# Performance work log

Measured on AMD Instinct MI355X. Metric: run time of the kernel, lower is better.

## Reference

```python
import jax, jax.numpy as jnp
import numpy as np

# ---- static config (mirrors init_kwargs + fixed setup box dims) ----
PC_MIN = jnp.array([0.0, -40.0, -3.0])
VOXEL_SIZE = jnp.array([0.05, 0.05, 0.1])
STRIDE = 4                     # pool_cfg.STRIDE and multi_scale_3d_strides['x_conv4']
EXTEND = 2.0                   # model_cfg.ROI_EXTEND_FACTOR
GRID_ZYX = (10, 400, 352)      # sparse spatial shape after stride-4 downsample [z,y,x]
# grid_size = round(extended_dims / voxel_size / STRIDE) for fixed dims [6.4,3.2,1.6]
GX, GY, GZ = 64, 32, 4
G = GX * GY * GZ
N_VOX, C = 200_000, 128
M = 64
KX, KY, KZ = 7, 7, 3


def setup_inputs() -> dict:
    key = jax.random.key(0)
    k1, k2, k3, k4, k5, k6, k7, k8, k9 = jax.random.split(key, 9)
    ctr = jnp.stack([
        jax.random.uniform(k1, (M,), minval=10.0, maxval=60.0),
        jax.random.uniform(k2, (M,), minval=-25.0, maxval=25.0),
        jax.random.uniform(k3, (M,), minval=-1.5, maxval=0.5)], axis=-1)
    dims = jnp.tile(jnp.array([[6.4, 3.2, 1.6]], jnp.float32), (M, 1))  # fixed -> static grid
    yaw = jax.random.uniform(k4, (M, 1), minval=-np.pi, maxval=np.pi)
    rois = jnp.concatenate([ctr, dims, yaw], axis=-1).astype(jnp.float32)
    proto_box = jnp.array([0.0, 0.0, 0.0, 6.4, 3.2, 1.6, 0.3], jnp.float32)
    voxel_feats = jax.random.normal(k5, (N_VOX, C), jnp.float32)
    feat_proto = jax.random.normal(k6, (1, KX, KY, KZ, C), jnp.float32) * 0.1
    zc = jax.random.randint(k7, (N_VOX,), 0, GRID_ZYX[0])
    yc = jax.random.randint(k8, (N_VOX,), 0, GRID_ZYX[1])
    xc = jax.random.randint(k9, (N_VOX,), 0, GRID_ZYX[2])
    voxel_coords = jnp.stack([jnp.zeros_like(zc), zc, yc, xc], -1).astype(jnp.int32)
    return dict(rois=rois, proto_box=proto_box, voxel_feats=voxel_feats,
                feat_proto=feat_proto, voxel_coords=voxel_coords)


def _dense_grid_points(box):
    # get_dense_grid_points: row-major (x,y,z) index order, matches torch nonzero()
    idx = jnp.stack(jnp.meshgrid(jnp.arange(GX), jnp.arange(GY), jnp.arange(GZ),
                                 indexing='ij'), -1).reshape(-1, 3).astype(jnp.float32)
    gs = jnp.array([GX, GY, GZ], jnp.float32)
    return (idx + 0.5) / gs * box[3:6] - box[3:6] / 2.0  # (G,3)


def _rotate_z(pts, ang):
    # common_utils.rotate_points_along_z: pts @ [[c,s,0],[-s,c,0],[0,0,1]]
    c, s = jnp.cos(ang), jnp.sin(ang)
    R = jnp.stack([jnp.stack([c, s, 0.0 * c]),
                   jnp.stack([-s, c, 0.0 * c]),
                   jnp.stack([0.0 * c, 0.0 * c, 1.0 + 0.0 * c])])
    return pts @ R


def reference(rois, proto_box, voxel_feats, feat_proto, voxel_coords):
    # generate_voxel2pinds: dense [Z,Y,X] grid of voxel row indices, -1 = empty
    v2p = -jnp.ones(GRID_ZYX, jnp.int32)
    v2p = v2p.at[voxel_coords[:, 1], voxel_coords[:, 2], voxel_coords[:, 3]].set(
        jnp.arange(N_VOX, dtype=jnp.int32))

    def per_roi(box):
        box = box.at[3:5].multiply(EXTEND)                 # xy_dim_extend
        local = _dense_grid_points(box)                    # (G,3)
        xyz = _rotate_z(local, box[6]) + box[:3]           # global roi grid points
        coords = jnp.floor((xyz - PC_MIN) / VOXEL_SIZE)    # '//' floor-div semantics
        coords = jnp.floor(coords / STRIDE).astype(jnp.int32)
        xc, yc, zc = coords[:, 0], coords[:, 1], coords[:, 2]
        inb = ((zc >= 0) & (zc < GRID_ZYX[0]) & (yc >= 0) & (yc < GRID_ZYX[1]) &
               (xc >= 0) & (xc < GRID_ZYX[2]))
        pidx = v2p[jnp.clip(zc, 0, GRID_ZYX[0] - 1),
                   jnp.clip(yc, 0, GRID_ZYX[1] - 1),
                   jnp.clip(xc, 0, GRID_ZYX[2] - 1)]
        valid = inb & (pidx >= 0)
        feat = jnp.where(valid[:, None], voxel_feats[jnp.clip(pidx, 0)], 0.0)  # (G,C)
        return feat, xyz

    feats, grid_xyz = jax.vmap(per_roi)(rois)              # (M,G,C), (M,G,3)
    vol = feats.reshape(M, GX, GY, GZ, C).transpose(0, 4, 1, 2, 3)   # NCDHW
    kern = feat_proto.transpose(0, 4, 1, 2, 3)                        # (1,C,KX,KY,KZ)
    pads = [(KX // 2,) * 2, (KY // 2,) * 2, (KZ // 2,) * 2]           # ceil((k-1)/2)
    mm = jax.lax.conv_general_dilated(vol, kern, (1, 1, 1), pads,
                                      dimension_numbers=('NCDHW', 'OIDHW', 'NCDHW'))
    # fresh BatchNorm3d(1) applied per-ROI (batch 1 each call): per-sample norm
    mu = jnp.mean(mm, axis=(1, 2, 3, 4), keepdims=True)
    var = jnp.var(mm, axis=(1, 2, 3, 4), keepdims=True)
    mm = (mm - mu) / jnp.sqrt(var + 1e-5)
    idx = jnp.minimum(jnp.argmax(mm.reshape(M, -1), axis=1), G - 1)
    sel = jnp.take_along_axis(grid_xyz, idx[:, None, None], axis=1)[:, 0, :]  # (M,3)
    rois_new = jnp.tile(proto_box[None], (M, 1))
    rois_new = rois_new.at[:, :3].set(sel)
    return rois_new
```

## Files before the change

### kernel.cpp

```cpp
#include <hip/hip_runtime.h>
#include <stdint.h>

#define GRID_Z 10
#define GRID_Y 400
#define GRID_X 352
#define NGRID (GRID_Z * GRID_Y * GRID_X)
#define NVOX 200000
#define CCH 128
#define MROI 64
#define GXD 64
#define GYD 32
#define GZD 4
#define GCELLS 8192
#define NTAPS 147
#define TROWS 32
#define NSLC 12
#define PITCH 136
#define NTT 10
#define BFRAGN (NTT * 4 * 64)
#define VCLR ((NGRID / 4 + 255) / 256)
#define ABLK 16

typedef short bf16x8 __attribute__((ext_vector_type(8)));
typedef float f32x4 __attribute__((ext_vector_type(4)));

__device__ __forceinline__ unsigned f2bf(float x) {
    unsigned u = __float_as_uint(x);
    return (u + 0x7FFFu + ((u >> 16) & 1u)) >> 16;
}
__device__ __forceinline__ float bf2f(unsigned h) {
    return __uint_as_float(h << 16);
}

__device__ __forceinline__ void cell_xyz(const float* __restrict__ roi, int g,
                                         float& X, float& Y, float& Z) {
#pragma clang fp contract(off)
    int iz = g & 3;
    int iy = (g >> 2) & 31;
    int ix = g >> 7;
    float bx = roi[3] * 2.0f;
    float by = roi[4] * 2.0f;
    float bz = roi[5];
    float lx = (ix + 0.5f) / 64.0f * bx - bx / 2.0f;
    float ly = (iy + 0.5f) / 32.0f * by - by / 2.0f;
    float lz = (iz + 0.5f) / 4.0f  * bz - bz / 2.0f;
    float c = cosf(roi[6]);
    float s = sinf(roi[6]);
    X = lx * c + ly * (-s) + roi[0];
    Y = lx * s + ly * c    + roi[1];
    Z = lz + roi[2];
}

__global__ void k_prep(const float* __restrict__ fproto, const float* __restrict__ rois,
                       uint4* __restrict__ bH, uint4* __restrict__ bL,
                       float2* __restrict__ rtrig, unsigned long long* __restrict__ best,
                       int* __restrict__ cnt, unsigned* __restrict__ done,
                       int* __restrict__ v2p) {
    if (blockIdx.x < NTT) {
        int tT   = blockIdx.x;
        int ks   = threadIdx.x >> 6;
        int lane = threadIdx.x & 63;
        int tap  = tT * 16 + (lane & 15);
        int k0   = ks * 32 + (lane >> 4) * 8;
        unsigned hi[8], lo[8];
        #pragma unroll
        for (int j = 0; j < 8; ++j) {
            float x = (tap < NTAPS) ? fproto[tap * CCH + k0 + j] : 0.0f;
            unsigned h = f2bf(x);
            float r = x - bf2f(h);
            hi[j] = h;
            lo[j] = f2bf(r);
        }
        uint4 uh, ul;
        uh.x = hi[0] | (hi[1] << 16); uh.y = hi[2] | (hi[3] << 16);
        uh.z = hi[4] | (hi[5] << 16); uh.w = hi[6] | (hi[7] << 16);
        ul.x = lo[0] | (lo[1] << 16); ul.y = lo[2] | (lo[3] << 16);
        ul.z = lo[4] | (lo[5] << 16); ul.w = lo[6] | (lo[7] << 16);
        int idx = (tT * 4 + ks) * 64 + lane;
        bH[idx] = uh;
        bL[idx] = ul;
    } else if (blockIdx.x == NTT) {
#pragma clang fp contract(off)
        int t = threadIdx.x;
        if (t < MROI) {
            float yaw = rois[t * 7 + 6];
            rtrig[t] = make_float2(cosf(yaw), sinf(yaw));
            cnt[t] = 0;
            best[t] = 0ull;
        }
        if (t == 0) *done = 0u;
    } else {
        int i = (blockIdx.x - NTT - 1) * 256 + threadIdx.x;
        if (i < NGRID / 4) {
            int4* p = (int4*)v2p;
            p[i] = make_int4(-1, -1, -1, -1);
        }
    }
}

__global__ void k_scatter(const int* __restrict__ vcoords, int* __restrict__ v2p) {
    int i = blockIdx.x * 256 + threadIdx.x;
    if (i >= NVOX) return;
    int z = vcoords[i * 4 + 1];
    int y = vcoords[i * 4 + 2];
    int x = vcoords[i * 4 + 3];
    atomicMax(&v2p[(z * GRID_Y + y) * GRID_X + x], i);
}

__global__ void k_build(const float* __restrict__ rois, const float2* __restrict__ rtrig,
                        const int* __restrict__ v2p, unsigned* __restrict__ list,
                        int* __restrict__ cnt) {
#pragma clang fp contract(off)
    int m   = blockIdx.y;
    int idx = blockIdx.x * 256 + threadIdx.x;
    int ix  = idx >> 5;
    int iy  = idx & 31;
    int lane = threadIdx.x & 63;

    const float* roi = rois + m * 7;
    float c = rtrig[m].x, s = rtrig[m].y;
    float bx = roi[3] * 2.0f;
    float by = roi[4] * 2.0f;
    float bz = roi[5];
    float lx = (ix + 0.5f) / 64.0f * bx - bx / 2.0f;
    float ly = (iy + 0.5f) / 32.0f * by - by / 2.0f;
    float X = lx * c + ly * (-s) + roi[0];
    float Y = lx * s + ly * c    + roi[1];
    float fx = floorf((X - 0.0f)     / 0.05f);
    float fy = floorf((Y - (-40.0f)) / 0.05f);
    int cx = (int)floorf(fx / 4.0f);
    int cy = (int)floorf(fy / 4.0f);
    bool okxy = (cy >= 0 && cy < GRID_Y && cx >= 0 && cx < GRID_X);
    int gbase = (ix << 7) | (iy << 2);

    #pragma unroll
    for (int iz = 0; iz < 4; ++iz) {
        float lz = (iz + 0.5f) / 4.0f * bz - bz / 2.0f;
        float Z  = lz + roi[2];
        float fz = floorf((Z - (-3.0f)) / 0.1f);
        int cz = (int)floorf(fz / 4.0f);
        int p = -1;
        if (okxy && cz >= 0 && cz < GRID_Z)
            p = v2p[(cz * GRID_Y + cy) * GRID_X + cx];
        bool v = p >= 0;
        unsigned long long bal = __ballot(v);
        int nset = __popcll(bal);
        int base = 0;
        if (lane == 0 && nset) base = atomicAdd(&cnt[m], nset);
        base = __shfl(base, 0, 64);
        if (v) {
            int pos = __popcll(bal & ((1ull << lane) - 1ull));
            list[m * GCELLS + base + pos] = ((unsigned)p << 13) | (unsigned)(gbase | iz);
        }
    }
}

__global__ __launch_bounds__(256) void k_dots(
        const float* __restrict__ vfeat, const uint4* __restrict__ bH,
        const uint4* __restrict__ bL, const unsigned* __restrict__ list,
        const int* __restrict__ cnt, float* __restrict__ partial) {
    __shared__ float sscore[GCELLS];
    __shared__ __align__(16) unsigned short sAh[TROWS * PITCH];
    __shared__ __align__(16) unsigned short sAl[TROWS * PITCH];
    __shared__ unsigned sg[TROWS];

    const int m    = blockIdx.y;
    const int tid  = threadIdx.x;
    const int w    = tid >> 6;
    const int lane = tid & 63;
    const int rt   = w >> 1;
    const int th   = w & 1;
    const int col  = lane & 15;
    const int kg   = lane >> 4;
    const int n    = cnt[m];
    const unsigned* lst = list + m * GCELLS;

    int tkx[5], tky[5], tkz[5], tok[5];
    #pragma unroll
    for (int tt = 0; tt < 5; ++tt) {
        int t = th * 80 + tt * 16 + col;
        tok[tt] = t < NTAPS;
        int tc = tok[tt] ? t : 0;
        int kx  = tc / 21;
        int rem = tc - kx * 21;
        tkx[tt] = kx; tky[tt] = rem / 3; tkz[tt] = rem - tky[tt] * 3;
    }
    {
        float4* s4 = (float4*)sscore;
        #pragma unroll
        for (int i = 0; i < GCELLS / 4 / 256; ++i)
            s4[tid + 256 * i] = make_float4(0.f, 0.f, 0.f, 0.f);
    }
    for (int vt0 = blockIdx.x * TROWS; vt0 < n; vt0 += TROWS * NSLC) {
        __syncthreads();
        {
            int r = tid >> 3, q = tid & 7, v = vt0 + r;
            unsigned e = 0xFFFFFFFFu;
            if (v < n) e = lst[v];
            if (q == 0) sg[r] = e;
            if (e != 0xFFFFFFFFu) {
                int p = (int)(e >> 13);
                const float4* src = (const float4*)(vfeat + (size_t)p * CCH) + q * 4;
                unsigned hb[16], lb[16];
                #pragma unroll
                for (int j = 0; j < 4; ++j) {
                    float4 s = src[j];
                    float xs[4] = {s.x, s.y, s.z, s.w};
                    #pragma unroll
                    for (int c = 0; c < 4; ++c) {
                        unsigned h = f2bf(xs[c]);
                        hb[j * 4 + c] = h;
                        lb[j * 4 + c] = f2bf(xs[c] - bf2f(h));
                    }
                }
                uint4 h0, h1, l0, l1;
                h0.x = hb[0]  | (hb[1]  << 16); h0.y = hb[2]  | (hb[3]  << 16);
                h0.z = hb[4]  | (hb[5]  << 16); h0.w = hb[6]  | (hb[7]  << 16);
                h1.x = hb[8]  | (hb[9]  << 16); h1.y = hb[10] | (hb[11] << 16);
                h1.z = hb[12] | (hb[13] << 16); h1.w = hb[14] | (hb[15] << 16);
                l0.x = lb[0]  | (lb[1]  << 16); l0.y = lb[2]  | (lb[3]  << 16);
                l0.z = lb[4]  | (lb[5]  << 16); l0.w = lb[6]  | (lb[7]  << 16);
                l1.x = lb[8]  | (lb[9]  << 16); l1.y = lb[10] | (lb[11] << 16);
                l1.z = lb[12] | (lb[13] << 16); l1.w = lb[14] | (lb[15] << 16);
                uint4* dh = (uint4*)((char*)sAh + r * (PITCH * 2) + q * 32);
                uint4* dl = (uint4*)((char*)sAl + r * (PITCH * 2) + q * 32);
                dh[0] = h0; dh[1] = h1;
                dl[0] = l0; dl[1] = l1;
            }
        }
        __syncthreads();
        bf16x8 ah[4], al[4];
        const char* abh = (const char*)sAh + (rt * 16 + col) * (PITCH * 2);
        const char* abl = (const char*)sAl + (rt * 16 + col) * (PITCH * 2);
        #pragma unroll
        for (int ks = 0; ks < 4; ++ks) {
            ah[ks] = *(const bf16x8*)(abh + ks * 64 + kg * 16);
            al[ks] = *(const bf16x8*)(abl + ks * 64 + kg * 16);
        }
        f32x4 acc[5];
        #pragma unroll
        for (int tt = 0; tt < 5; ++tt) acc[tt] = (f32x4){0.f, 0.f, 0.f, 0.f};
        #pragma unroll
        for (int tt = 0; tt < 5; ++tt) {
            const int bi = ((th * 5 + tt) * 4) * 64 + lane;
            #pragma unroll
            for (int ks = 0; ks < 4; ++ks) {
                uint4 uh = bH[bi + ks * 64];
                uint4 ul = bL[bi + ks * 64];
                bf16x8 bh = *(bf16x8*)&uh;
                bf16x8 bl = *(bf16x8*)&ul;
                acc[tt] = __builtin_amdgcn_mfma_f32_16x16x32_bf16(ah[ks], bh, acc[tt], 0, 0, 0);
                acc[tt] = __builtin_amdgcn_mfma_f32_16x16x32_bf16(ah[ks], bl, acc[tt], 0, 0, 0);
                acc[tt] = __builtin_amdgcn_mfma_f32_16x16x32_bf16(al[ks], bh, acc[tt], 0, 0, 0);
            }
        }
        #pragma unroll
        for (int tt = 0; tt < 5; ++tt) {
            if (!tok[tt]) continue;
            #pragma unroll
            for (int rg = 0; rg < 4; ++rg) {
                unsigned e = sg[rt * 16 + kg * 4 + rg];
                if (e == 0xFFFFFFFFu) continue;
                int g  = (int)(e & 8191u);
                int cx = (g >> 7)        - (tkx[tt] - 3);
                int cy = ((g >> 2) & 31) - (tky[tt] - 3);
                int cz = (g & 3)         - (tkz[tt] - 1);
                if ((unsigned)cx < (unsigned)GXD && (unsigned)cy < (unsigned)GYD &&
                    (unsigned)cz < (unsigned)GZD)
                    atomicAdd(&sscore[(cx << 7) | (cy << 2) | cz], acc[tt][rg]);
            }
        }
    }
    __syncthreads();
    {
        float* dst = partial + ((size_t)m * NSLC + blockIdx.x) * GCELLS;
        const float4* s4 = (const float4*)sscore;
        float4* d4 = (float4*)dst;
        #pragma unroll
        for (int i = 0; i < GCELLS / 4 / 256; ++i)
            d4[tid + 256 * i] = s4[tid + 256 * i];
    }
}

__global__ __launch_bounds__(256) void k_argfin(
        const float* __restrict__ partial, const float* __restrict__ rois,
        const float* __restrict__ pbox, unsigned long long* __restrict__ best,
        unsigned* __restrict__ done, float* __restrict__ out) {
    __shared__ unsigned long long red[256];
    __shared__ unsigned lastflag;
    const int tid = threadIdx.x;
    const int m = blockIdx.y;
    const float* base = partial + (size_t)m * NSLC * GCELLS;
    const int c0 = blockIdx.x * (GCELLS / ABLK);
    unsigned long long bk = 0ull;
    #pragma unroll
    for (int i = 0; i < GCELLS / ABLK / 256; ++i) {
        int c = c0 + tid + 256 * i;
        float v = 0.0f;
        #pragma unroll
        for (int s = 0; s < NSLC; ++s) v += base[s * GCELLS + c];
        unsigned ub  = __float_as_uint(v);
        unsigned key = (ub & 0x80000000u) ? ~ub : (ub | 0x80000000u);
        unsigned long long pk =
            ((unsigned long long)key << 32) | (unsigned)(GCELLS - 1 - c);
        bk = bk > pk ? bk : pk;
    }
    red[tid] = bk;
    __syncthreads();
    for (int st = 128; st > 0; st >>= 1) {
        if (tid < st) {
            unsigned long long o = red[tid + st];
            if (o > red[tid]) red[tid] = o;
        }
        __syncthreads();
    }
    if (tid == 0) {
        atomicMax(&best[m], red[0]);
        __threadfence();
        unsigned d = atomicAdd(done, 1u);
        lastflag = (d == ABLK * MROI - 1u);
    }
    __syncthreads();
    if (lastflag && tid < MROI) {
        unsigned long long bv = atomicMax(&best[tid], 0ull);
        int g = (GCELLS - 1) - (int)(unsigned)(bv & 0xFFFFFFFFu);
        float X, Y, Z;
        cell_xyz(rois + tid * 7, g, X, Y, Z);
        out[tid * 7 + 0] = X;
        out[tid * 7 + 1] = Y;
        out[tid * 7 + 2] = Z;
        out[tid * 7 + 3] = pbox[3];
        out[tid * 7 + 4] = pbox[4];
        out[tid * 7 + 5] = pbox[5];
        out[tid * 7 + 6] = pbox[6];
    }
}

extern "C" void kernel_launch(void* const* d_in, const int* in_sizes, int n_in,
                              void* d_out, int out_size, void* d_ws, size_t ws_size,
                              hipStream_t stream) {
    const float* rois    = (const float*)d_in[0];
    const float* pbox    = (const float*)d_in[1];
    const float* vfeat   = (const float*)d_in[2];
    const float* fproto  = (const float*)d_in[3];
    const int*   vcoords = (const int*)d_in[4];
    float* out = (float*)d_out;

    int*      v2p     = (int*)d_ws;
    unsigned* list    = (unsigned*)(v2p + NGRID);
    float*    partial = (float*)(list + (size_t)MROI * GCELLS);
    uint4*    bH      = (uint4*)(partial + (size_t)NSLC * MROI * GCELLS);
    uint4*    bL      = bH + BFRAGN;
    float2*   rtrig   = (float2*)(bL + BFRAGN);
    unsigned long long* best = (unsigned long long*)(rtrig + MROI);
    int*      cnt     = (int*)(best + MROI);
    unsigned* done    = (unsigned*)(cnt + MROI);

    k_prep   <<<NTT + 1 + VCLR, 256, 0, stream>>>(fproto, rois, bH, bL, rtrig,
                                                  best, cnt, done, v2p);
    k_scatter<<<(NVOX + 255) / 256, 256, 0, stream>>>(vcoords, v2p);
    k_build  <<<dim3(8, MROI), 256, 0, stream>>>(rois, rtrig, v2p, list, cnt);
    k_dots   <<<dim3(NSLC, MROI), 256, 0, stream>>>(vfeat, bH, bL, list, cnt, partial);
    k_argfin <<<dim3(ABLK, MROI), 256, 0, stream>>>(partial, rois, pbox, best, done, out);
}
```

Measured before the change: 283.0 us.

## Replicate B-fragment weights across workspace and split MFMA accumulator chains

The prep kernel now writes up to 32 copies of the bf16 hi/lo prototype fragments into the workspace, and each k_dots block reads the copy picked by its block index. This is meant to spread many blocks' reads of the same small weight buffer over different addresses and cache lines, easing hot-spotting in L2 or across channels. The three dependent MFMAs per step are also split into two accumulators (hi*hi and the cross terms), which shortens the dependency chain, and the two are summed before the shared-memory atomic. The cost is more prep writes, more workspace, and a slightly different summation order.

```diff
diff --git a/kernel.cpp b/kernel.cpp
--- a/kernel.cpp
+++ b/kernel.cpp
@@ -55,7 +55,7 @@
                        uint4* __restrict__ bH, uint4* __restrict__ bL,
                        float2* __restrict__ rtrig, unsigned long long* __restrict__ best,
                        int* __restrict__ cnt, unsigned* __restrict__ done,
-                       int* __restrict__ v2p) {
+                       int* __restrict__ v2p, int rep) {
     if (blockIdx.x < NTT) {
         int tT   = blockIdx.x;
         int ks   = threadIdx.x >> 6;
@@ -77,8 +77,10 @@
         ul.x = lo[0] | (lo[1] << 16); ul.y = lo[2] | (lo[3] << 16);
         ul.z = lo[4] | (lo[5] << 16); ul.w = lo[6] | (lo[7] << 16);
         int idx = (tT * 4 + ks) * 64 + lane;
-        bH[idx] = uh;
-        bL[idx] = ul;
+        for (int r = 0; r < rep; ++r) {
+            bH[r * BFRAGN + idx] = uh;
+            bL[r * BFRAGN + idx] = ul;
+        }
     } else if (blockIdx.x == NTT) {
 #pragma clang fp contract(off)
         int t = threadIdx.x;
@@ -158,7 +160,7 @@
 __global__ __launch_bounds__(256) void k_dots(
         const float* __restrict__ vfeat, const uint4* __restrict__ bH,
         const uint4* __restrict__ bL, const unsigned* __restrict__ list,
-        const int* __restrict__ cnt, float* __restrict__ partial) {
+        const int* __restrict__ cnt, float* __restrict__ partial, int rpmask) {
     __shared__ float sscore[GCELLS];
     __shared__ __align__(16) unsigned short sAh[TROWS * PITCH];
     __shared__ __align__(16) unsigned short sAl[TROWS * PITCH];
@@ -174,6 +176,10 @@
     const int kg   = lane >> 4;
     const int n    = cnt[m];
     const unsigned* lst = list + m * GCELLS;
+
+    const int rp = (blockIdx.y * NSLC + blockIdx.x) & rpmask;
+    const uint4* __restrict__ bHp = bH + rp * BFRAGN;
+    const uint4* __restrict__ bLp = bL + rp * BFRAGN;
 
     int tkx[5], tky[5], tkz[5], tok[5];
     #pragma unroll
@@ -237,21 +243,24 @@
             ah[ks] = *(const bf16x8*)(abh + ks * 64 + kg * 16);
             al[ks] = *(const bf16x8*)(abl + ks * 64 + kg * 16);
         }
-        f32x4 acc[5];
-        #pragma unroll
-        for (int tt = 0; tt < 5; ++tt) acc[tt] = (f32x4){0.f, 0.f, 0.f, 0.f};
+        f32x4 accH[5], accL[5];
+        #pragma unroll
+        for (int tt = 0; tt < 5; ++tt) {
+            accH[tt] = (f32x4){0.f, 0.f, 0.f, 0.f};
+            accL[tt] = (f32x4){0.f, 0.f, 0.f, 0.f};
+        }
         #pragma unroll
         for (int tt = 0; tt < 5; ++tt) {
             const int bi = ((th * 5 + tt) * 4) * 64 + lane;
             #pragma unroll
             for (int ks = 0; ks < 4; ++ks) {
-                uint4 uh = bH[bi + ks * 64];
-                uint4 ul = bL[bi + ks * 64];
+                uint4 uh = bHp[bi + ks * 64];
+                uint4 ul = bLp[bi + ks * 64];
                 bf16x8 bh = *(bf16x8*)&uh;
                 bf16x8 bl = *(bf16x8*)&ul;
-                acc[tt] = __builtin_amdgcn_mfma_f32_16x16x32_bf16(ah[ks], bh, acc[tt], 0, 0, 0);
-                acc[tt] = __builtin_amdgcn_mfma_f32_16x16x32_bf16(ah[ks], bl, acc[tt], 0, 0, 0);
-                acc[tt] = __builtin_amdgcn_mfma_f32_16x16x32_bf16(al[ks], bh, acc[tt], 0, 0, 0);
+                accH[tt] = __builtin_amdgcn_mfma_f32_16x16x32_bf16(ah[ks], bh, accH[tt], 0, 0, 0);
+                accL[tt] = __builtin_amdgcn_mfma_f32_16x16x32_bf16(ah[ks], bl, accL[tt], 0, 0, 0);
+                accL[tt] = __builtin_amdgcn_mfma_f32_16x16x32_bf16(al[ks], bh, accL[tt], 0, 0, 0);
             }
         }
         #pragma unroll
@@ -267,7 +276,8 @@
                 int cz = (g & 3)         - (tkz[tt] - 1);
                 if ((unsigned)cx < (unsigned)GXD && (unsigned)cy < (unsigned)GYD &&
                     (unsigned)cz < (unsigned)GZD)
-                    atomicAdd(&sscore[(cx << 7) | (cy << 2) | cz], acc[tt][rg]);
+                    atomicAdd(&sscore[(cx << 7) | (cy << 2) | cz],
+                              accH[tt][rg] + accL[tt][rg]);
             }
         }
     }
@@ -346,20 +356,29 @@
     const int*   vcoords = (const int*)d_in[4];
     float* out = (float*)d_out;
 
+    size_t fixedB = ((size_t)NGRID + (size_t)MROI * GCELLS +
+                     (size_t)NSLC * MROI * GCELLS) * 4;
+    size_t tailB  = (size_t)MROI * (8 + 8 + 4) + 64;
+    int rep = 32;
+    while (rep > 1 &&
+           fixedB + (size_t)rep * BFRAGN * 2 * sizeof(uint4) + tailB > ws_size)
+        rep >>= 1;
+
     int*      v2p     = (int*)d_ws;
     unsigned* list    = (unsigned*)(v2p + NGRID);
     float*    partial = (float*)(list + (size_t)MROI * GCELLS);
     uint4*    bH      = (uint4*)(partial + (size_t)NSLC * MROI * GCELLS);
-    uint4*    bL      = bH + BFRAGN;
-    float2*   rtrig   = (float2*)(bL + BFRAGN);
+    uint4*    bL      = bH + (size_t)rep * BFRAGN;
+    float2*   rtrig   = (float2*)(bL + (size_t)rep * BFRAGN);
     unsigned long long* best = (unsigned long long*)(rtrig + MROI);
     int*      cnt     = (int*)(best + MROI);
     unsigned* done    = (unsigned*)(cnt + MROI);
 
     k_prep   <<<NTT + 1 + VCLR, 256, 0, stream>>>(fproto, rois, bH, bL, rtrig,
-                                                  best, cnt, done, v2p);
+                                                  best, cnt, done, v2p, rep);
     k_scatter<<<(NVOX + 255) / 256, 256, 0, stream>>>(vcoords, v2p);
     k_build  <<<dim3(8, MROI), 256, 0, stream>>>(rois, rtrig, v2p, list, cnt);
-    k_dots   <<<dim3(NSLC, MROI), 256, 0, stream>>>(vfeat, bH, bL, list, cnt, partial);
+    k_dots   <<<dim3(NSLC, MROI), 256, 0, stream>>>(vfeat, bH, bL, list, cnt,
+                                                    partial, rep - 1);
     k_argfin <<<dim3(ABLK, MROI), 256, 0, stream>>>(partial, rois, pbox, best, done, out);
 }
```

New measurement: 285.7 us. About the same (+0.9%).
